# Performance work log

Measured on AMD Instinct MI355X. Metric: run time of the kernel, lower is better.

## Reference

```python
import jax, jax.numpy as jnp
import numpy as np

N, E, B = 100000, 800000, 64
IN, HC1, HC2, NC, SA = 256, 128, 32, 2, 350
NEG = 0.2  # GATv2Conv default negative_slope


def forward(s_x, s_edge_index, s_batch, s_root_n_id,
            Wq, bq, Wk, bk, Wv, bv,
            Wl1, bl1, Wr1, br1, att1, bias1,
            Wl2, bl2, Wr2, br2, att2, bias2,
            Wl3, bl3, Wr3, br3, att3, bias3,
            c1w, c1b, c2W, c2b, c3W, c3b,
            linW, linb, aW1, ab1, aW2, mW1, mb1, mW2, mb2):
    src, dst = s_edge_index[0], s_edge_index[1]
    x_info = s_x
    # --- SelfAttention over seq_len=1 (x.unsqueeze(1)) ---
    z = s_x[:, None, :]                                   # [N,1,IN]
    q = z @ Wq + bq; k = z @ Wk + bk; v = z @ Wv + bv      # [N,1,SA]
    scores = jnp.einsum('nqd,nkd->nqk', q, k) / jnp.sqrt(jnp.float32(SA))
    probs = jax.nn.softmax(scores, axis=-1)
    h = jnp.einsum('nqk,nkd->nqd', probs, v)[:, 0, :]      # [N,SA]

    def gatv2(x, Wl, bl, Wr, br, att, bias):
        # PyG GATv2Conv, heads=1, eval mode (dropout off)
        xl = x @ Wl + bl                                   # source transform [N,O]
        xr = x @ Wr + br                                   # target transform [N,O]
        e = jax.nn.leaky_relu(xl[src] + xr[dst], NEG)      # [E,O]
        s = e @ att                                        # [E]
        smax = jax.ops.segment_max(s, dst, num_segments=N)
        smax = jnp.where(jnp.isfinite(smax), smax, 0.0)
        ex = jnp.exp(s - smax[dst])
        den = jax.ops.segment_sum(ex, dst, num_segments=N)
        alpha = ex / jnp.maximum(den[dst], 1e-16)
        return jax.ops.segment_sum(alpha[:, None] * xl[src], dst, num_segments=N) + bias

    h = jax.nn.relu(gatv2(h, Wl1, bl1, Wr1, br1, att1, bias1))
    h = jax.nn.relu(gatv2(h, Wl2, bl2, Wr2, br2, att2, bias2))
    h = jax.nn.relu(gatv2(h, Wl3, bl3, Wr3, br3, att3, bias3))   # [N,HC2]

    # --- readout: root node feature ++ global mean pool ---
    cnt = jax.ops.segment_sum(jnp.ones((N,), h.dtype), s_batch, num_segments=B)
    pooled = jax.ops.segment_sum(h, s_batch, num_segments=B) / jnp.maximum(cnt, 1.0)[:, None]
    sx = jnp.concatenate([h[s_root_n_id], pooled], axis=-1)       # [B,2*HC2]

    # --- info branch on raw root features ---
    info = x_info[s_root_n_id]                                    # [B,IN]
    info = c1w[0] * info[:, :-2] + c1w[1] * info[:, 1:-1] + c1w[2] * info[:, 2:] + c1b  # Conv1d(1,1,3)
    t = info.T                                                    # [IN-2,B]
    t = jax.nn.relu(c2W @ t + c2b[:, None])                       # [HC1,B]
    t = jax.nn.relu(c3W @ t + c3b[:, None])                       # [HC1//2,B]
    t = t.T                                                       # [B,HC1//2]
    L = t.shape[1]
    t = jax.nn.relu(t.reshape(B, HC2, L // HC2).mean(-1))         # AdaptiveAvgPool1d(HC2)

    sx = jax.nn.relu(sx @ linW + linb)                            # [B,HC2]

    # --- semantic attention over the two views ---
    emb = jnp.stack([sx, t], axis=1)                              # [B,2,HC2]
    w = jnp.tanh(emb @ aW1 + ab1) @ aW2                           # [B,2,1]
    beta = jax.nn.softmax(w, axis=1)
    emb = (beta * emb).sum(1)                                     # [B,HC2]

    return jax.nn.softmax(jnp.tanh(emb @ mW1 + mb1) @ mW2 + mb2, axis=1)  # [B,NC]


def setup_inputs() -> dict:
    keys = iter(jax.random.split(jax.random.key(0), 64))
    def nrm(*shape):
        return jax.random.normal(next(keys), shape, dtype=jnp.float32) * 0.05
    inp = {}
    inp['s_x'] = jax.random.normal(next(keys), (N, IN), dtype=jnp.float32)
    inp['s_edge_index'] = jax.random.randint(next(keys), (2, E), 0, N)
    inp['s_batch'] = jnp.sort(jax.random.randint(next(keys), (N,), 0, B))
    inp['s_root_n_id'] = jax.random.randint(next(keys), (B,), 0, N)
    inp['Wq'] = nrm(IN, SA); inp['bq'] = nrm(SA)
    inp['Wk'] = nrm(IN, SA); inp['bk'] = nrm(SA)
    inp['Wv'] = nrm(IN, SA); inp['bv'] = nrm(SA)
    inp['Wl1'] = nrm(SA, HC1); inp['bl1'] = nrm(HC1)
    inp['Wr1'] = nrm(SA, HC1); inp['br1'] = nrm(HC1)
    inp['att1'] = nrm(HC1); inp['bias1'] = nrm(HC1)
    inp['Wl2'] = nrm(HC1, HC1 // 2); inp['bl2'] = nrm(HC1 // 2)
    inp['Wr2'] = nrm(HC1, HC1 // 2); inp['br2'] = nrm(HC1 // 2)
    inp['att2'] = nrm(HC1 // 2); inp['bias2'] = nrm(HC1 // 2)
    inp['Wl3'] = nrm(HC1 // 2, HC2); inp['bl3'] = nrm(HC2)
    inp['Wr3'] = nrm(HC1 // 2, HC2); inp['br3'] = nrm(HC2)
    inp['att3'] = nrm(HC2); inp['bias3'] = nrm(HC2)
    inp['c1w'] = nrm(3); inp['c1b'] = nrm(1)
    inp['c2W'] = nrm(HC1, IN - 2); inp['c2b'] = nrm(HC1)
    inp['c3W'] = nrm(HC1 // 2, HC1); inp['c3b'] = nrm(HC1 // 2)
    inp['linW'] = nrm(2 * HC2, HC2); inp['linb'] = nrm(HC2)
    inp['aW1'] = nrm(HC2, 16); inp['ab1'] = nrm(16); inp['aW2'] = nrm(16, 1)
    inp['mW1'] = nrm(HC2, 16); inp['mb1'] = nrm(16)
    inp['mW2'] = nrm(16, NC); inp['mb2'] = nrm(NC)
    return inp


def reference(s_x, s_edge_index, s_batch, s_root_n_id,
              Wq, bq, Wk, bk, Wv, bv,
              Wl1, bl1, Wr1, br1, att1, bias1,
              Wl2, bl2, Wr2, br2, att2, bias2,
              Wl3, bl3, Wr3, br3, att3, bias3,
              c1w, c1b, c2W, c2b, c3W, c3b,
              linW, linb, aW1, ab1, aW2, mW1, mb1, mW2, mb2):
    return forward(s_x, s_edge_index, s_batch, s_root_n_id,
                   Wq, bq, Wk, bk, Wv, bv,
                   Wl1, bl1, Wr1, br1, att1, bias1,
                   Wl2, bl2, Wr2, br2, att2, bias2,
                   Wl3, bl3, Wr3, br3, att3, bias3,
                   c1w, c1b, c2W, c2b, c3W, c3b,
                   linW, linb, aW1, ab1, aW2, mW1, mb1, mW2, mb2)
```

## Files before the change

### kernel.cpp

```cpp
#include <hip/hip_runtime.h>
#include <hip/hip_bf16.h>
#include <math.h>

typedef unsigned short ushort_t;
typedef __attribute__((ext_vector_type(8))) short bfrag;
typedef __attribute__((ext_vector_type(4))) float ffrag;

#define GLOBAL_AS __attribute__((address_space(1)))
#define LDS_AS    __attribute__((address_space(3)))

constexpr int N_NODES = 100000;
constexpr int N_EDGES = 800000;
constexpr int NB      = 64;
constexpr int IN_F    = 256;
constexpr int HC1C    = 128;
constexpr int HC2C    = 32;
constexpr int SA_D    = 350;
constexpr float NEG   = 0.2f;

constexpr int SCAN_NBLK = (N_NODES + 255) / 256;
constexpr int MB64      = (N_NODES + 63) / 64;

constexpr size_t OFF_WT1    = 0;
constexpr size_t OFF_WT2    = OFF_WT1 + 65536;
constexpr size_t OFF_WT3    = OFF_WT2 + 16384;
constexpr size_t OFF_BC1    = OFF_WT3 + 4096;
constexpr size_t OFF_BC2    = OFF_BC1 + 256;
constexpr size_t OFF_BC3    = OFF_BC2 + 128;
constexpr size_t OFF_XLR    = OFF_BC3 + 64;
constexpr size_t OFF_H      = OFF_XLR + (size_t)N_NODES * 256;
constexpr size_t OFF_DEG    = OFF_H + (size_t)N_NODES * 128;
constexpr size_t OFF_ROWPTR = OFF_DEG + N_NODES;
constexpr size_t OFF_CURSOR = OFF_ROWPTR + N_NODES + 1;
constexpr size_t OFF_BLKS   = OFF_CURSOR + N_NODES;
constexpr size_t OFF_BLKO   = OFF_BLKS + 512;
constexpr size_t OFF_CSRSRC = OFF_BLKO + 512;
constexpr size_t OFF_POOLED = OFF_CSRSRC + N_EDGES;
constexpr size_t OFF_CNT    = OFF_POOLED + NB * HC2C;
constexpr size_t WS_FLOATS  = OFF_CNT + NB;

__device__ __forceinline__ ushort_t f2bf(float f) {
  union { float f; unsigned int u; } a;
  a.f = f;
  unsigned int r = a.u + 0x7FFFu + ((a.u >> 16) & 1u);
  return (ushort_t)(r >> 16);
}
__device__ __forceinline__ float bf2f(ushort_t h) {
  union { unsigned int u; float f; } a;
  a.u = ((unsigned int)h) << 16;
  return a.f;
}
__device__ __forceinline__ float2 bfp(unsigned int u) {
  float2 r;
  r.x = __uint_as_float(u << 16);
  r.y = __uint_as_float(u & 0xFFFF0000u);
  return r;
}
__device__ __forceinline__ unsigned int pack2(float a, float b) {
  unsigned int ua = __float_as_uint(a);
  ua += 0x7FFFu + ((ua >> 16) & 1u);
  unsigned int ub = __float_as_uint(b);
  ub += 0x7FFFu + ((ub >> 16) & 1u);
  return __builtin_amdgcn_perm(ub, ua, 0x07060302u);
}
__device__ __forceinline__ void unp8(uint4 u, float* x) {
  float2 p0 = bfp(u.x), p1 = bfp(u.y), p2 = bfp(u.z), p3 = bfp(u.w);
  x[0] = p0.x; x[1] = p0.y; x[2] = p1.x; x[3] = p1.y;
  x[4] = p2.x; x[5] = p2.y; x[6] = p3.x; x[7] = p3.y;
}

__global__ void k_pack_all(const float* __restrict__ Wv, const float* __restrict__ bv,
                           const float* __restrict__ Wl1, const float* __restrict__ bl1,
                           const float* __restrict__ Wr1, const float* __restrict__ br1,
                           const float* __restrict__ Wl2, const float* __restrict__ bl2,
                           const float* __restrict__ Wr2, const float* __restrict__ br2,
                           const float* __restrict__ Wl3, const float* __restrict__ bl3,
                           const float* __restrict__ Wr3, const float* __restrict__ br3,
                           ushort_t* __restrict__ WT1, float* __restrict__ bc1,
                           ushort_t* __restrict__ WT2, float* __restrict__ bc2,
                           ushort_t* __restrict__ WT3, float* __restrict__ bc3) {
  int blk = blockIdx.x;
  int tid = threadIdx.x;
  if (blk < 256) {
    int t = blk * 256 + tid;
    int n = t & 255, k = t >> 8;
    const float* Wx = (n < 128) ? Wl1 : Wr1;
    int j = n & 127;
    float a = 0.f;
    for (int kk = 0; kk < SA_D; ++kk) a += Wv[k * SA_D + kk] * Wx[kk * 128 + j];
    WT1[(size_t)n * 256 + k] = f2bf(a);
  } else if (blk == 256) {
    int n = tid;
    const float* Wx = (n < 128) ? Wl1 : Wr1;
    const float* bx = (n < 128) ? bl1 : br1;
    int j = n & 127;
    float a = bx[j];
    for (int kk = 0; kk < SA_D; ++kk) a += bv[kk] * Wx[kk * 128 + j];
    bc1[n] = a;
  } else if (blk < 321) {
    int t = (blk - 257) * 256 + tid;
    int n = t & 127, k = t >> 7;
    if (t < 128) bc2[t] = (t < 64) ? bl2[t] : br2[t - 64];
    float v = (n < 64) ? Wl2[k * 64 + n] : Wr2[k * 64 + (n - 64)];
    WT2[(size_t)n * 128 + k] = f2bf(v);
  } else {
    int t = (blk - 321) * 256 + tid;
    int n = t & 63, k = t >> 6;
    if (t < 64) bc3[t] = (t < 32) ? bl3[t] : br3[t - 32];
    float v = (n < 32) ? Wl3[k * 32 + n] : Wr3[k * 32 + (n - 32)];
    WT3[(size_t)n * 64 + k] = f2bf(v);
  }
}

__global__ void k_hist(const int* __restrict__ dst, int* __restrict__ deg) {
  int e = blockIdx.x * blockDim.x + threadIdx.x;
  if (e < N_EDGES) atomicAdd(deg + dst[e], 1);
}

__global__ void k_scan_local(const int* __restrict__ deg, int* __restrict__ row_ptr,
                             int* __restrict__ blk_sum) {
  __shared__ int sh[256];
  int t = threadIdx.x;
  int i = blockIdx.x * 256 + t;
  int v = (i < N_NODES) ? deg[i] : 0;
  sh[t] = v;
  __syncthreads();
  for (int off = 1; off < 256; off <<= 1) {
    int add = (t >= off) ? sh[t - off] : 0;
    __syncthreads();
    sh[t] += add;
    __syncthreads();
  }
  if (i < N_NODES) row_ptr[i] = sh[t] - v;
  if (t == 255) blk_sum[blockIdx.x] = sh[255];
}

__global__ void k_scan_blk(const int* __restrict__ blk_sum, int* __restrict__ blk_off) {
  __shared__ int sh[512];
  int t = threadIdx.x;
  int v = (t < SCAN_NBLK) ? blk_sum[t] : 0;
  sh[t] = v;
  __syncthreads();
  for (int off = 1; off < 512; off <<= 1) {
    int add = (t >= off) ? sh[t - off] : 0;
    __syncthreads();
    sh[t] += add;
    __syncthreads();
  }
  blk_off[t] = sh[t] - v;
}

__global__ void k_scan_add(int* __restrict__ row_ptr, const int* __restrict__ blk_off,
                           int* __restrict__ cursor) {
  int i = blockIdx.x * blockDim.x + threadIdx.x;
  if (i < N_NODES) {
    int v = row_ptr[i] + blk_off[i >> 8];
    row_ptr[i] = v;
    cursor[i] = v;
  }
  if (i == 0) row_ptr[N_NODES] = N_EDGES;
}

__global__ void k_fill(const int* __restrict__ src, const int* __restrict__ dst,
                       int* __restrict__ cursor, int* __restrict__ csr_src) {
  int e = blockIdx.x * blockDim.x + threadIdx.x;
  if (e >= N_EDGES) return;
  int pos = atomicAdd(cursor + dst[e], 1);
  csr_src[pos] = src[e];
}

template <int K, int NN, int BN, bool AF32>
__global__ __launch_bounds__(256, 4) void k_gemm_bf16(const void* __restrict__ xin,
                                                      const ushort_t* __restrict__ WT,
                                                      const float* __restrict__ bc,
                                                      ushort_t* __restrict__ out, int M) {
  constexpr int BM  = 64;
  constexpr int RT  = 2;
  constexpr int CT  = BN / 32;
  constexpr int NK  = K / 32;
  constexpr int GPR = K / 8;
  __shared__ __align__(16) ushort_t As[BM * K];

  const int tid  = threadIdx.x;
  const int wave = tid >> 6;
  const int lane = tid & 63;
  const int quad = lane >> 4;
  const int l16  = lane & 15;
  const int wrow = wave & 1;
  const int wcol = wave >> 1;
  const int m0   = blockIdx.x * BM;
  const int n0   = blockIdx.y * BN;
  const int nb   = n0 + wcol * (BN / 2);

  const float*    af32 = (const float*)xin;
  const ushort_t* ab16 = (const ushort_t*)xin;

  bfrag bcur[CT], bnxt[CT];
#pragma unroll
  for (int ct = 0; ct < CT; ++ct)
    bcur[ct] = *(const bfrag*)(WT + (size_t)(nb + ct * 16 + l16) * K + quad * 8);

  if (AF32) {
    float4 av[16];
#pragma unroll
    for (int j = 0; j < 16; ++j) {
      const int r = wave * 16 + j;
      int m = m0 + r;
      if (m >= M) m = M - 1;
      av[j] = *(const float4*)(af32 + (size_t)m * K + lane * 4);
    }
#pragma unroll
    for (int j = 0; j < 16; ++j) {
      const int r = wave * 16 + j;
      uint2 pk;
      pk.x = pack2(av[j].x, av[j].y);
      pk.y = pack2(av[j].z, av[j].w);
      *(uint2*)&As[(size_t)r * K + (((lane >> 1) ^ (r & 7)) * 8) + (lane & 1) * 4] = pk;
    }
  } else {
    constexpr int NI = GPR / 4;
#pragma unroll
    for (int j = 0; j < NI; ++j) {
      const int s0 = (wave * NI + j) * 64;
      const int s  = s0 + lane;
      const int r  = s / GPR;
      const int c  = s & (GPR - 1);
      int m = m0 + r;
      if (m >= M) m = M - 1;
      const ushort_t* srcp = ab16 + (size_t)m * K + (size_t)(c ^ (r & 7)) * 8;
      __builtin_amdgcn_global_load_lds((const GLOBAL_AS unsigned int*)srcp,
                                       (LDS_AS unsigned int*)&As[(size_t)s0 * 8], 16, 0, 0);
    }
  }

  ffrag acc[RT][CT];
#pragma unroll
  for (int rt = 0; rt < RT; ++rt)
#pragma unroll
    for (int ct = 0; ct < CT; ++ct) acc[rt][ct] = ffrag{0.f, 0.f, 0.f, 0.f};

  __syncthreads();

#pragma unroll
  for (int ks = 0; ks < NK; ++ks) {
    if (ks + 1 < NK) {
#pragma unroll
      for (int ct = 0; ct < CT; ++ct)
        bnxt[ct] = *(const bfrag*)(WT + (size_t)(nb + ct * 16 + l16) * K + (ks + 1) * 32 + quad * 8);
    }
    bfrag a[RT];
#pragma unroll
    for (int rt = 0; rt < RT; ++rt) {
      const int r = wrow * 32 + rt * 16 + l16;
      a[rt] = *(const bfrag*)&As[(size_t)r * K + (size_t)(((ks * 4 + quad) ^ (r & 7)) * 8)];
    }
#pragma unroll
    for (int ct = 0; ct < CT; ++ct)
#pragma unroll
      for (int rt = 0; rt < RT; ++rt)
        acc[rt][ct] = __builtin_amdgcn_mfma_f32_16x16x32_bf16(a[rt], bcur[ct], acc[rt][ct], 0, 0, 0);
    if (ks + 1 < NK) {
#pragma unroll
      for (int ct = 0; ct < CT; ++ct) bcur[ct] = bnxt[ct];
    }
  }

#pragma unroll
  for (int rt = 0; rt < RT; ++rt)
#pragma unroll
    for (int ct = 0; ct < CT; ++ct) {
      const int n = nb + ct * 16 + l16;
      const float bb = bc[n];
#pragma unroll
      for (int r = 0; r < 4; ++r) {
        const int m = m0 + wrow * 32 + rt * 16 + quad * 4 + r;
        if (m < M) out[(size_t)m * NN + n] = f2bf(acc[rt][ct][r] + bb);
      }
    }
}

template <int C>
__global__ void k_gat(const ushort_t* __restrict__ xlr, const int* __restrict__ row_ptr,
                      const int* __restrict__ csr_src, const float* __restrict__ att,
                      const float* __restrict__ bias, ushort_t* __restrict__ h) {
  constexpr int G = C / 8;
  constexpr int RS = 2 * C;
  int t = blockIdx.x * blockDim.x + threadIdx.x;
  int d = t / G;
  int lane = t - d * G;
  if (d >= N_NODES) return;
  float xr[8], a[8];
  unp8(*(const uint4*)(xlr + (size_t)d * RS + C + lane * 8), xr);
  *(float4*)&a[0] = *(const float4*)(att + lane * 8);
  *(float4*)&a[4] = *(const float4*)(att + lane * 8 + 4);
  float acc[8];
#pragma unroll
  for (int j = 0; j < 8; ++j) acc[j] = 0.f;
  float den = 0.f;
  const int e0 = row_ptr[d], e1 = row_ptr[d + 1];
  int i = e0;
  for (; i + 4 <= e1; i += 4) {
    uint4 u[4];
#pragma unroll
    for (int q = 0; q < 4; ++q)
      u[q] = *(const uint4*)(xlr + (size_t)csr_src[i + q] * RS + lane * 8);
    float xl[4][8];
#pragma unroll
    for (int q = 0; q < 4; ++q) unp8(u[q], xl[q]);
    float p[4] = {0.f, 0.f, 0.f, 0.f};
#pragma unroll
    for (int j = 0; j < 8; ++j) {
#pragma unroll
      for (int q = 0; q < 4; ++q) {
        float v = xl[q][j] + xr[j];
        v = v > 0.f ? v : NEG * v;
        p[q] += a[j] * v;
      }
    }
#pragma unroll
    for (int off = G / 2; off > 0; off >>= 1) {
#pragma unroll
      for (int q = 0; q < 4; ++q) p[q] += __shfl_xor(p[q], off, 64);
    }
    float ex[4];
#pragma unroll
    for (int q = 0; q < 4; ++q) ex[q] = expf(p[q]);
    den += (ex[0] + ex[1]) + (ex[2] + ex[3]);
#pragma unroll
    for (int j = 0; j < 8; ++j)
      acc[j] += (ex[0] * xl[0][j] + ex[1] * xl[1][j]) + (ex[2] * xl[2][j] + ex[3] * xl[3][j]);
  }
  for (; i < e1; ++i) {
    int s = csr_src[i];
    float xl[8];
    unp8(*(const uint4*)(xlr + (size_t)s * RS + lane * 8), xl);
    float p = 0.f;
#pragma unroll
    for (int j = 0; j < 8; ++j) {
      float v = xl[j] + xr[j];
      v = v > 0.f ? v : NEG * v;
      p += a[j] * v;
    }
#pragma unroll
    for (int off = G / 2; off > 0; off >>= 1) p += __shfl_xor(p, off, 64);
    float ex = expf(p);
    den += ex;
#pragma unroll
    for (int j = 0; j < 8; ++j) acc[j] += ex * xl[j];
  }
  float inv = 1.f / fmaxf(den, 1e-16f);
  float o[8];
#pragma unroll
  for (int j = 0; j < 8; ++j)
    o[j] = fmaxf(acc[j] * inv + bias[lane * 8 + j], 0.f);
  uint4 pk;
  pk.x = pack2(o[0], o[1]);
  pk.y = pack2(o[2], o[3]);
  pk.z = pack2(o[4], o[5]);
  pk.w = pack2(o[6], o[7]);
  *(uint4*)(h + (size_t)d * C + lane * 8) = pk;
}

__global__ void k_pool(const ushort_t* __restrict__ h3, const int* __restrict__ batch,
                       float* __restrict__ pooled, float* __restrict__ cnt) {
  constexpr int NPB = 1024;
  constexpr int NPT = NPB / 8;
  int c = threadIdx.x & 31;
  int r = threadIdx.x >> 5;
  int base = blockIdx.x * NPB + r * NPT;
  if (base >= N_NODES) return;
  int end = base + NPT;
  if (end > N_NODES) end = N_NODES;
  int cur_b = batch[base];
  float acc = 0.f, count = 0.f;
  for (int n = base; n < end; ++n) {
    int b = batch[n];
    if (b != cur_b) {
      atomicAdd(pooled + cur_b * HC2C + c, acc);
      if (c == 0) atomicAdd(cnt + cur_b, count);
      cur_b = b;
      acc = 0.f;
      count = 0.f;
    }
    acc += bf2f(h3[(size_t)n * HC2C + c]);
    count += 1.f;
  }
  atomicAdd(pooled + cur_b * HC2C + c, acc);
  if (c == 0) atomicAdd(cnt + cur_b, count);
}

__global__ __launch_bounds__(256) void k_tail(
    const ushort_t* __restrict__ h3, const int* __restrict__ root,
    const float* __restrict__ pooled, const float* __restrict__ cnt,
    const float* __restrict__ linW, const float* __restrict__ linb,
    const float* __restrict__ X, const float* __restrict__ c1w,
    const float* __restrict__ c1b, const float* __restrict__ c2W,
    const float* __restrict__ c2b, const float* __restrict__ c3W,
    const float* __restrict__ c3b, const float* __restrict__ aW1,
    const float* __restrict__ ab1, const float* __restrict__ aW2,
    const float* __restrict__ mW1, const float* __restrict__ mb1,
    const float* __restrict__ mW2, const float* __restrict__ mb2,
    float* __restrict__ out) {
  constexpr int L = IN_F - 2;
  __shared__ float s_info[L];
  __shared__ float s_t1[HC1C];
  __shared__ float s_t2[HC1C / 2];
  __shared__ float s_e0[HC2C];
  __shared__ float s_e1[HC2C];
  const int b = blockIdx.x;
  const int tid = threadIdx.x;
  const int r = root[b];
  const float* xr = X + (size_t)r * IN_F;
  for (int i = tid; i < L; i += 256)
    s_info[i] = c1w[0] * xr[i] + c1w[1] * xr[i + 1] + c1w[2] * xr[i + 2] + c1b[0];
  __syncthreads();
  if (tid < HC1C) {
    float a = c2b[tid];
    for (int i = 0; i < L; ++i) a += c2W[tid * L + i] * s_info[i];
    s_t1[tid] = fmaxf(a, 0.f);
  }
  __syncthreads();
  if (tid < HC1C / 2) {
    float a = c3b[tid];
    for (int i = 0; i < HC1C; ++i) a += c3W[tid * HC1C + i] * s_t1[i];
    s_t2[tid] = fmaxf(a, 0.f);
  }
  __syncthreads();
  if (tid < HC2C) {
    float v = 0.5f * (s_t2[2 * tid] + s_t2[2 * tid + 1]);
    s_e1[tid] = fmaxf(v, 0.f);
  } else if (tid < 2 * HC2C) {
    int j = tid - HC2C;
    float inv = 1.f / fmaxf(cnt[b], 1.f);
    float a = linb[j];
    for (int c = 0; c < HC2C; ++c) a += bf2f(h3[(size_t)r * HC2C + c]) * linW[c * HC2C + j];
    for (int c = 0; c < HC2C; ++c) a += pooled[b * HC2C + c] * inv * linW[(HC2C + c) * HC2C + j];
    s_e0[j] = fmaxf(a, 0.f);
  }
  __syncthreads();
  if (tid == 0) {
    float w0 = 0.f, w1 = 0.f;
    for (int j = 0; j < 16; ++j) {
      float z0 = ab1[j], z1 = ab1[j];
      for (int c = 0; c < HC2C; ++c) {
        z0 += s_e0[c] * aW1[c * 16 + j];
        z1 += s_e1[c] * aW1[c * 16 + j];
      }
      w0 += tanhf(z0) * aW2[j];
      w1 += tanhf(z1) * aW2[j];
    }
    float mx = fmaxf(w0, w1);
    float x0 = expf(w0 - mx), x1 = expf(w1 - mx);
    float inv = 1.f / (x0 + x1);
    float b0 = x0 * inv, b1 = x1 * inv;
    float l0 = mb2[0], l1 = mb2[1];
    for (int j = 0; j < 16; ++j) {
      float z = mb1[j];
      for (int c = 0; c < HC2C; ++c) z += (b0 * s_e0[c] + b1 * s_e1[c]) * mW1[c * 16 + j];
      float tz = tanhf(z);
      l0 += tz * mW2[j * 2 + 0];
      l1 += tz * mW2[j * 2 + 1];
    }
    float m2 = fmaxf(l0, l1);
    float y0 = expf(l0 - m2), y1 = expf(l1 - m2);
    float is = 1.f / (y0 + y1);
    out[b * 2 + 0] = y0 * is;
    out[b * 2 + 1] = y1 * is;
  }
}

extern "C" void kernel_launch(void* const* d_in, const int* in_sizes, int n_in, void* d_out,
                              int out_size, void* d_ws, size_t ws_size, hipStream_t stream) {
  if (ws_size < WS_FLOATS * sizeof(float)) return;

  const float* s_x   = (const float*)d_in[0];
  const int*   edge  = (const int*)d_in[1];
  const int*   batch = (const int*)d_in[2];
  const int*   root  = (const int*)d_in[3];
  const float* Wv    = (const float*)d_in[8];
  const float* bv    = (const float*)d_in[9];
  const float* Wl1   = (const float*)d_in[10];
  const float* bl1   = (const float*)d_in[11];
  const float* Wr1   = (const float*)d_in[12];
  const float* br1   = (const float*)d_in[13];
  const float* att1  = (const float*)d_in[14];
  const float* bias1 = (const float*)d_in[15];
  const float* Wl2   = (const float*)d_in[16];
  const float* bl2   = (const float*)d_in[17];
  const float* Wr2   = (const float*)d_in[18];
  const float* br2   = (const float*)d_in[19];
  const float* att2  = (const float*)d_in[20];
  const float* bias2 = (const float*)d_in[21];
  const float* Wl3   = (const float*)d_in[22];
  const float* bl3   = (const float*)d_in[23];
  const float* Wr3   = (const float*)d_in[24];
  const float* br3   = (const float*)d_in[25];
  const float* att3  = (const float*)d_in[26];
  const float* bias3 = (const float*)d_in[27];
  const float* c1w   = (const float*)d_in[28];
  const float* c1b   = (const float*)d_in[29];
  const float* c2W   = (const float*)d_in[30];
  const float* c2b   = (const float*)d_in[31];
  const float* c3W   = (const float*)d_in[32];
  const float* c3b   = (const float*)d_in[33];
  const float* linW  = (const float*)d_in[34];
  const float* linb  = (const float*)d_in[35];
  const float* aW1   = (const float*)d_in[36];
  const float* ab1   = (const float*)d_in[37];
  const float* aW2   = (const float*)d_in[38];
  const float* mW1   = (const float*)d_in[39];
  const float* mb1   = (const float*)d_in[40];
  const float* mW2   = (const float*)d_in[41];
  const float* mb2   = (const float*)d_in[42];

  const int* src = edge;
  const int* dst = edge + N_EDGES;

  float*    ws      = (float*)d_ws;
  ushort_t* WT1     = (ushort_t*)(ws + OFF_WT1);
  ushort_t* WT2     = (ushort_t*)(ws + OFF_WT2);
  ushort_t* WT3     = (ushort_t*)(ws + OFF_WT3);
  float*    bc1     = ws + OFF_BC1;
  float*    bc2     = ws + OFF_BC2;
  float*    bc3     = ws + OFF_BC3;
  ushort_t* xlr     = (ushort_t*)(ws + OFF_XLR);
  ushort_t* hbuf    = (ushort_t*)(ws + OFF_H);
  int*      deg     = (int*)(ws + OFF_DEG);
  int*      row_ptr = (int*)(ws + OFF_ROWPTR);
  int*      cursor  = (int*)(ws + OFF_CURSOR);
  int*      blks    = (int*)(ws + OFF_BLKS);
  int*      blko    = (int*)(ws + OFF_BLKO);
  int*      csr_src = (int*)(ws + OFF_CSRSRC);
  float*    pooled  = ws + OFF_POOLED;
  float*    cnt     = ws + OFF_CNT;
  float*    out     = (float*)d_out;

  hipMemsetAsync(deg, 0, N_NODES * sizeof(int), stream);
  k_hist<<<(N_EDGES + 255) / 256, 256, 0, stream>>>(dst, deg);
  k_scan_local<<<SCAN_NBLK, 256, 0, stream>>>(deg, row_ptr, blks);
  k_scan_blk<<<1, 512, 0, stream>>>(blks, blko);
  k_scan_add<<<SCAN_NBLK, 256, 0, stream>>>(row_ptr, blko, cursor);
  k_fill<<<(N_EDGES + 255) / 256, 256, 0, stream>>>(src, dst, cursor, csr_src);

  k_pack_all<<<337, 256, 0, stream>>>(Wv, bv, Wl1, bl1, Wr1, br1, Wl2, bl2, Wr2, br2, Wl3,
                                      bl3, Wr3, br3, WT1, bc1, WT2, bc2, WT3, bc3);

  k_gemm_bf16<256, 256, 128, true><<<dim3(MB64, 2), 256, 0, stream>>>(s_x, WT1, bc1, xlr,
                                                                      N_NODES);
  k_gat<128><<<(N_NODES * 16 + 255) / 256, 256, 0, stream>>>(xlr, row_ptr, csr_src, att1,
                                                             bias1, hbuf);

  k_gemm_bf16<128, 128, 128, false><<<dim3(MB64, 1), 256, 0, stream>>>(hbuf, WT2, bc2, xlr,
                                                                       N_NODES);
  k_gat<64><<<(N_NODES * 8 + 255) / 256, 256, 0, stream>>>(xlr, row_ptr, csr_src, att2,
                                                           bias2, hbuf);

  k_gemm_bf16<64, 64, 64, false><<<dim3(MB64, 1), 256, 0, stream>>>(hbuf, WT3, bc3, xlr,
                                                                    N_NODES);
  k_gat<32><<<(N_NODES * 4 + 255) / 256, 256, 0, stream>>>(xlr, row_ptr, csr_src, att3,
                                                           bias3, hbuf);

  hipMemsetAsync(pooled, 0, (NB * HC2C + NB) * sizeof(float), stream);
  k_pool<<<(N_NODES + 1023) / 1024, 256, 0, stream>>>(hbuf, batch, pooled, cnt);
  k_tail<<<NB, 256, 0, stream>>>(hbuf, root, pooled, cnt, linW, linb, s_x, c1w, c1b, c2W,
                                 c2b, c3W, c3b, aW1, ab1, aW2, mW1, mb1, mW2, mb2, out);
}
```

Baseline: 659.4 us.

## Pipeline GEMM K-loop with double-buffered LDS tiles for A and B

```diff
diff --git a/kernel.cpp b/kernel.cpp
--- a/kernel.cpp
+++ b/kernel.cpp
@@ -5,9 +5,6 @@
 typedef unsigned short ushort_t;
 typedef __attribute__((ext_vector_type(8))) short bfrag;
 typedef __attribute__((ext_vector_type(4))) float ffrag;
-
-#define GLOBAL_AS __attribute__((address_space(1)))
-#define LDS_AS    __attribute__((address_space(3)))
 
 constexpr int N_NODES = 100000;
 constexpr int N_EDGES = 800000;
@@ -174,64 +171,88 @@
                                                       const ushort_t* __restrict__ WT,
                                                       const float* __restrict__ bc,
                                                       ushort_t* __restrict__ out, int M) {
-  constexpr int BM  = 64;
   constexpr int RT  = 2;
   constexpr int CT  = BN / 32;
   constexpr int NK  = K / 32;
-  constexpr int GPR = K / 8;
-  __shared__ __align__(16) ushort_t As[BM * K];
+  constexpr int BGT = BN / 64;
+  constexpr int BUS = 2048 + BN * 32;
+  __shared__ __align__(16) ushort_t lds[2][BUS];
 
   const int tid  = threadIdx.x;
   const int wave = tid >> 6;
   const int lane = tid & 63;
   const int quad = lane >> 4;
   const int l16  = lane & 15;
-  const int wrow = wave & 1;
-  const int wcol = wave >> 1;
-  const int m0   = blockIdx.x * BM;
+  const int wrow = wave >> 1;
+  const int wcol = wave & 1;
+  const int m0   = blockIdx.x * 64;
   const int n0   = blockIdx.y * BN;
-  const int nb   = n0 + wcol * (BN / 2);
 
   const float*    af32 = (const float*)xin;
   const ushort_t* ab16 = (const ushort_t*)xin;
 
-  bfrag bcur[CT], bnxt[CT];
-#pragma unroll
-  for (int ct = 0; ct < CT; ++ct)
-    bcur[ct] = *(const bfrag*)(WT + (size_t)(nb + ct * 16 + l16) * K + quad * 8);
-
-  if (AF32) {
-    float4 av[16];
-#pragma unroll
-    for (int j = 0; j < 16; ++j) {
-      const int r = wave * 16 + j;
-      int m = m0 + r;
-      if (m >= M) m = M - 1;
-      av[j] = *(const float4*)(af32 + (size_t)m * K + lane * 4);
-    }
-#pragma unroll
-    for (int j = 0; j < 16; ++j) {
-      const int r = wave * 16 + j;
-      uint2 pk;
-      pk.x = pack2(av[j].x, av[j].y);
-      pk.y = pack2(av[j].z, av[j].w);
-      *(uint2*)&As[(size_t)r * K + (((lane >> 1) ^ (r & 7)) * 8) + (lane & 1) * 4] = pk;
-    }
-  } else {
-    constexpr int NI = GPR / 4;
-#pragma unroll
-    for (int j = 0; j < NI; ++j) {
-      const int s0 = (wave * NI + j) * 64;
-      const int s  = s0 + lane;
-      const int r  = s / GPR;
-      const int c  = s & (GPR - 1);
-      int m = m0 + r;
-      if (m >= M) m = M - 1;
-      const ushort_t* srcp = ab16 + (size_t)m * K + (size_t)(c ^ (r & 7)) * 8;
-      __builtin_amdgcn_global_load_lds((const GLOBAL_AS unsigned int*)srcp,
-                                       (LDS_AS unsigned int*)&As[(size_t)s0 * 8], 16, 0, 0);
-    }
-  }
+  const int aline = tid >> 3, alg = tid & 7;
+  const int arow  = aline * 2 + (alg >> 2);
+  int am = m0 + arow;
+  if (am >= M) am = M - 1;
+  const size_t aoff = (size_t)am * K + (alg & 3) * 8;
+  const int awi = aline * 64 + ((alg ^ (aline & 7)) * 8);
+
+  size_t boff[BGT];
+  int    bwi[BGT];
+#pragma unroll
+  for (int g = 0; g < BGT; ++g) {
+    const int sB = g * 256 + tid;
+    const int bline = sB >> 3, blg = sB & 7;
+    const int brow = bline * 2 + (blg >> 2);
+    boff[g] = (size_t)(n0 + brow) * K + (blg & 3) * 8;
+    bwi[g]  = 2048 + bline * 64 + ((blg ^ (bline & 7)) * 8);
+  }
+
+  int ard[RT];
+#pragma unroll
+  for (int rt = 0; rt < RT; ++rt) {
+    const int row = wrow * 32 + rt * 16 + l16;
+    const int line = row >> 1;
+    ard[rt] = line * 64 + ((((row & 1) * 4 + quad) ^ (line & 7)) * 8);
+  }
+  int brd[CT];
+#pragma unroll
+  for (int ct = 0; ct < CT; ++ct) {
+    const int rowb = wcol * (BN / 2) + ct * 16 + l16;
+    const int lineb = rowb >> 1;
+    brd[ct] = 2048 + lineb * 64 + ((((rowb & 1) * 4 + quad) ^ (lineb & 7)) * 8);
+  }
+
+  float4 sf[2][2];
+  uint4  sh[2];
+  uint4  sb[2][BGT];
+
+  auto LOAD = [&](int ks, int s) {
+    if (AF32) {
+      sf[s][0] = *(const float4*)(af32 + aoff + (size_t)ks * 32);
+      sf[s][1] = *(const float4*)(af32 + aoff + (size_t)ks * 32 + 4);
+    } else {
+      sh[s] = *(const uint4*)(ab16 + aoff + (size_t)ks * 32);
+    }
+#pragma unroll
+    for (int g = 0; g < BGT; ++g)
+      sb[s][g] = *(const uint4*)(WT + boff[g] + (size_t)ks * 32);
+  };
+  auto WRITE = [&](int s, int b) {
+    uint4 w;
+    if (AF32) {
+      w.x = pack2(sf[s][0].x, sf[s][0].y);
+      w.y = pack2(sf[s][0].z, sf[s][0].w);
+      w.z = pack2(sf[s][1].x, sf[s][1].y);
+      w.w = pack2(sf[s][1].z, sf[s][1].w);
+    } else {
+      w = sh[s];
+    }
+    *(uint4*)&lds[b][awi] = w;
+#pragma unroll
+    for (int g = 0; g < BGT; ++g) *(uint4*)&lds[b][bwi[g]] = sb[s][g];
+  };
 
   ffrag acc[RT][CT];
 #pragma unroll
@@ -239,29 +260,27 @@
 #pragma unroll
     for (int ct = 0; ct < CT; ++ct) acc[rt][ct] = ffrag{0.f, 0.f, 0.f, 0.f};
 
-  __syncthreads();
-
-#pragma unroll
-  for (int ks = 0; ks < NK; ++ks) {
-    if (ks + 1 < NK) {
-#pragma unroll
-      for (int ct = 0; ct < CT; ++ct)
-        bnxt[ct] = *(const bfrag*)(WT + (size_t)(nb + ct * 16 + l16) * K + (ks + 1) * 32 + quad * 8);
-    }
+  LOAD(0, 0);
+  if (NK > 1) LOAD(1, 1);
+  WRITE(0, 0);
+  __syncthreads();
+
+#pragma unroll
+  for (int i = 0; i < NK; ++i) {
+    if (i + 2 < NK) LOAD(i + 2, i & 1);
     bfrag a[RT];
 #pragma unroll
-    for (int rt = 0; rt < RT; ++rt) {
-      const int r = wrow * 32 + rt * 16 + l16;
-      a[rt] = *(const bfrag*)&As[(size_t)r * K + (size_t)(((ks * 4 + quad) ^ (r & 7)) * 8)];
-    }
-#pragma unroll
-    for (int ct = 0; ct < CT; ++ct)
+    for (int rt = 0; rt < RT; ++rt) a[rt] = *(const bfrag*)&lds[i & 1][ard[rt]];
+#pragma unroll
+    for (int ct = 0; ct < CT; ++ct) {
+      bfrag bf = *(const bfrag*)&lds[i & 1][brd[ct]];
 #pragma unroll
       for (int rt = 0; rt < RT; ++rt)
-        acc[rt][ct] = __builtin_amdgcn_mfma_f32_16x16x32_bf16(a[rt], bcur[ct], acc[rt][ct], 0, 0, 0);
-    if (ks + 1 < NK) {
-#pragma unroll
-      for (int ct = 0; ct < CT; ++ct) bcur[ct] = bnxt[ct];
+        acc[rt][ct] = __builtin_amdgcn_mfma_f32_16x16x32_bf16(a[rt], bf, acc[rt][ct], 0, 0, 0);
+    }
+    if (i + 1 < NK) {
+      WRITE((i + 1) & 1, (i + 1) & 1);
+      __syncthreads();
     }
   }
 
@@ -269,7 +288,7 @@
   for (int rt = 0; rt < RT; ++rt)
 #pragma unroll
     for (int ct = 0; ct < CT; ++ct) {
-      const int n = nb + ct * 16 + l16;
+      const int n = n0 + wcol * (BN / 2) + ct * 16 + l16;
       const float bb = bc[n];
 #pragma unroll
       for (int r = 0; r < 4; ++r) {
```

After: 680.2 us. 1.03x slower.
